# Performance work log

Hardware: AMD Instinct MI355X
Metric: run time of the kernel (lower is better)

The kernel has to match this reference:

```python
import jax, jax.numpy as jnp
import numpy as np

B, Q, D = 4, 8, 128  # batch of volumes, poses per volume, volume side (L == D)


def setup_inputs() -> dict:
    key = jax.random.key(0)
    k1, k2 = jax.random.split(key)
    density = jax.random.normal(k1, (B, D, D, D), dtype=jnp.float32)
    rotation = jax.random.normal(k2, (B, Q, 3, 3), dtype=jnp.float32)
    return {"density": density, "rotation": rotation}


def _project(density, rotation):
    """density: (B, NZ, NY, NX); rotation: (B, Q, 3, 3) -> (B, Q, NY, NX).

    Replicates: rotate an L^3 coord grid, F.grid_sample (trilinear,
    align_corners=True, zero padding), then sum over the last grid axis.
    """
    b, NZ, NY, NX = density.shape
    q = rotation.shape[1]
    L = NZ  # module asserts D == NZ == NY == NX and uses L == D

    lin = jnp.linspace(-1.0, 1.0, L, dtype=density.dtype)
    xx, yy, zz = jnp.meshgrid(lin, lin, lin, indexing="ij")
    coords = jnp.stack([xx, yy, zz], axis=-1)  # (L, L, L, 3)

    Rf = rotation.reshape(b * q, 3, 3)
    # rot_coords[n,i,j,k,m] = sum_c coords[i,j,k,c] * R[n,c,m]
    rc = jnp.einsum("ijkc,ncm->nijkm", coords, Rf)  # (BQ, L, L, L, 3)

    # grid_sample convention: last dim is (x, y, z) indexing (NX, NY, NZ).
    # align_corners=True unnormalization: idx = (c + 1) / 2 * (size - 1)
    x = (rc[..., 0] + 1.0) * 0.5 * (NX - 1)
    y = (rc[..., 1] + 1.0) * 0.5 * (NY - 1)
    z = (rc[..., 2] + 1.0) * 0.5 * (NZ - 1)

    x0 = jnp.floor(x).astype(jnp.int32)
    y0 = jnp.floor(y).astype(jnp.int32)
    z0 = jnp.floor(z).astype(jnp.int32)
    fx = x - x0
    fy = y - y0
    fz = z - z0

    vol = jnp.broadcast_to(density[:, None], (b, q, NZ, NY, NX))
    vol_flat = vol.reshape(b * q, NZ * NY * NX)

    def corner(xc, yc, zc, w):
        valid = (xc >= 0) & (xc < NX) & (yc >= 0) & (yc < NY) & (zc >= 0) & (zc < NZ)
        xi = jnp.clip(xc, 0, NX - 1)
        yi = jnp.clip(yc, 0, NY - 1)
        zi = jnp.clip(zc, 0, NZ - 1)
        idx = (zi * NY + yi) * NX + xi  # (BQ, L, L, L)
        v = jnp.take_along_axis(vol_flat, idx.reshape(b * q, -1), axis=1)
        v = v.reshape(idx.shape)
        return jnp.where(valid, v, 0.0) * w

    sampled = (
        corner(x0,     y0,     z0,     (1 - fx) * (1 - fy) * (1 - fz))
        + corner(x0 + 1, y0,     z0,     fx * (1 - fy) * (1 - fz))
        + corner(x0,     y0 + 1, z0,     (1 - fx) * fy * (1 - fz))
        + corner(x0 + 1, y0 + 1, z0,     fx * fy * (1 - fz))
        + corner(x0,     y0,     z0 + 1, (1 - fx) * (1 - fy) * fz)
        + corner(x0 + 1, y0,     z0 + 1, fx * (1 - fy) * fz)
        + corner(x0,     y0 + 1, z0 + 1, (1 - fx) * fy * fz)
        + corner(x0 + 1, y0 + 1, z0 + 1, fx * fy * fz)
    )  # (BQ, L, L, L) over grid axes (X, Y, Z)

    sampled = sampled.reshape(b, q, L, L, L)
    proj = jnp.sum(sampled.transpose(0, 1, 3, 2, 4), axis=-1)  # (B, Q, L, L)
    return proj


def reference(density, rotation):
    return _project(density, rotation)
```

## Files before the change

kernel.cpp:

```cpp
#include <hip/hip_runtime.h>


#define LSZ 128
#define PACKED_BYTES ((size_t)4 * 128 * 128 * 128 * 8)

typedef unsigned int u4v __attribute__((ext_vector_type(4), aligned(8)));
typedef _Float16 h2 __attribute__((ext_vector_type(2)));

__device__ __forceinline__ h2 ash2(unsigned int u) {
    union { unsigned int u; h2 h; } c; c.u = u; return c.h;
}
__device__ __forceinline__ float dot2(unsigned int pair, h2 w, float acc) {
    return __builtin_amdgcn_fdot2(ash2(pair), w, acc, false);
}
__device__ __forceinline__ h2 pkw(float lo, float hi) {
    auto t = __builtin_amdgcn_cvt_pkrtz(lo, hi);
    union { decltype(t) a; h2 b; } c; c.a = t; return c.b;
}
__device__ __forceinline__ unsigned int pkh(float lo, float hi) {
    auto t = __builtin_amdgcn_cvt_pkrtz(lo, hi);
    union { decltype(t) a; unsigned int u; } c; c.a = t; return c.u;
}

__global__ __launch_bounds__(256) void pack_kernel(
    const float* __restrict__ density, uint2* __restrict__ packed)
{
    const int t  = blockIdx.x * 256 + threadIdx.x;
    const int xq = (t & 31) << 2;
    const int y  = (t >> 5) & 127;
    const int z  = (t >> 12) & 127;
    const int b  = t >> 19;
    const float* __restrict__ v = density + ((size_t)b << 21);
    const int y1 = min(y + 1, 127), z1 = min(z + 1, 127);
    const float4 a0 = *(const float4*)(v + (z  << 14) + (y  << 7) + xq);
    const float4 a1 = *(const float4*)(v + (z  << 14) + (y1 << 7) + xq);
    const float4 c0 = *(const float4*)(v + (z1 << 14) + (y  << 7) + xq);
    const float4 c1 = *(const float4*)(v + (z1 << 14) + (y1 << 7) + xq);
    uint4 o0, o1;
    o0.x = pkh(a0.x, a1.x); o0.y = pkh(c0.x, c1.x);
    o0.z = pkh(a0.y, a1.y); o0.w = pkh(c0.y, c1.y);
    o1.x = pkh(a0.z, a1.z); o1.y = pkh(c0.z, c1.z);
    o1.z = pkh(a0.w, a1.w); o1.w = pkh(c0.w, c1.w);
    uint4* dst = (uint4*)(packed + ((size_t)b << 21) + (z << 14) + (y << 7) + xq);
    dst[0] = o0; dst[1] = o1;
}

#define FPREPI(S, kk) do {                                                    \
    const float kf_ = (float)min((kk), d);                                    \
    const float X_ = fmaf(kf_, R20, Ax);                                      \
    const float Y_ = fmaf(kf_, R21, Ay);                                      \
    const float Z_ = fmaf(kf_, R22, Az);                                      \
    const int ix_ = (int)X_;                                                  \
    const int iy_ = (int)Y_;                                                  \
    const int iz_ = (int)Z_;                                                  \
    fx##S = __builtin_amdgcn_fractf(X_);                                      \
    const float fy_ = __builtin_amdgcn_fractf(Y_);                            \
    fz##S = __builtin_amdgcn_fractf(Z_);                                      \
    hy##S = pkw(1.0f - fy_, fy_);                                             \
    u##S = *(const u4v*)(vol2 + ((iz_ << 14) + (iy_ << 7) + ix_));            \
} while (0)

#define FCONSI(S) do {                                                        \
    const float gx0 = 1.0f - fx##S;                                           \
    const float gz0 = 1.0f - fz##S;                                           \
    const float m00 = dot2(u##S.x, hy##S, 0.0f);                 \
    const float m01 = dot2(u##S.y, hy##S, 0.0f);                 \
    const float m10 = dot2(u##S.z, hy##S, 0.0f);                 \
    const float m11 = dot2(u##S.w, hy##S, 0.0f);                 \
    const float s0_ = fmaf(gx0, m00, fx##S * m10);                            \
    const float s1_ = fmaf(gx0, m01, fx##S * m11);                            \
    acc = fmaf(gz0, s0_, fmaf(fz##S, s1_, acc));                              \
} while (0)

#define SPREP(S, kk) do {                                                     \
    const float kf_ = (float)(kk);                                            \
    const float X_ = fmaf(kf_, R20, Ax);                                      \
    const float Y_ = fmaf(kf_, R21, Ay);                                      \
    const float Z_ = fmaf(kf_, R22, Az);                                      \
    const int ix_ = (int)floorf(X_);                                          \
    const int iy_ = (int)floorf(Y_);                                          \
    const int iz_ = (int)floorf(Z_);                                          \
    const int ex_ = min(max(ix_, 0), 126);                                    \
    const int ey_ = min(max(iy_, 0), 126);                                    \
    const int ez_ = min(max(iz_, 0), 126);                                    \
    u##S = *(const u4v*)(vol2 + ((ez_ << 14) + (ey_ << 7) + ex_));            \
} while (0)

#define SCONS(S, kk) do {                                                     \
    const float kf_ = (float)(kk);                                            \
    const float X_ = fmaf(kf_, R20, Ax);                                      \
    const float Y_ = fmaf(kf_, R21, Ay);                                      \
    const float Z_ = fmaf(kf_, R22, Az);                                      \
    const float xf_ = floorf(X_), yf_ = floorf(Y_), zf_ = floorf(Z_);         \
    const int ix_ = (int)xf_, iy_ = (int)yf_, iz_ = (int)zf_;                 \
    const float fx_ = X_ - xf_, fy_ = Y_ - yf_, fz_ = Z_ - zf_;               \
    const bool vx0_ = (ix_ >= 0)  & (ix_ <= 127);                             \
    const bool vx1_ = (ix_ >= -1) & (ix_ <= 126);                             \
    const bool vy0_ = (iy_ >= 0)  & (iy_ <= 127);                             \
    const bool vy1_ = (iy_ >= -1) & (iy_ <= 126);                             \
    const bool vz0_ = (iz_ >= 0)  & (iz_ <= 127);                             \
    const bool vz1_ = (iz_ >= -1) & (iz_ <= 126);                             \
    const float gx0 = vx0_ ? (1.0f - fx_) : 0.0f;                             \
    const float gx1 = vx1_ ? fx_ : 0.0f;                                      \
    const float gy0 = vy0_ ? (1.0f - fy_) : 0.0f;                             \
    const float gy1 = vy1_ ? fy_ : 0.0f;                                      \
    const float gz0 = vz0_ ? (1.0f - fz_) : 0.0f;                             \
    const float gz1 = vz1_ ? fz_ : 0.0f;                                      \
    const bool xhi_ = (ix_ > 126), xlo_ = (ix_ < 0);                          \
    const bool yhi_ = (iy_ > 126), ylo_ = (iy_ < 0);                          \
    const bool zhi_ = (iz_ > 126), zlo_ = (iz_ < 0);                          \
    const float wlo_ = ylo_ ? gy1 : (yhi_ ? 0.0f : gy0);                      \
    const float whi_ = yhi_ ? gy0 : (ylo_ ? 0.0f : gy1);                      \
    const h2 hy_ = pkw(wlo_, whi_);                                           \
    const unsigned int a0z0 = xhi_ ? u##S.z : u##S.x;                         \
    const unsigned int a0z1 = xhi_ ? u##S.w : u##S.y;                         \
    const unsigned int a1z0 = xlo_ ? u##S.x : u##S.z;                         \
    const unsigned int a1z1 = xlo_ ? u##S.y : u##S.w;                         \
    const unsigned int dA = zhi_ ? a0z1 : a0z0;                  \
    const unsigned int dB = zlo_ ? a0z0 : a0z1;                  \
    const unsigned int dC = zhi_ ? a1z1 : a1z0;                  \
    const unsigned int dD = zlo_ ? a1z0 : a1z1;                  \
    const float m00 = dot2(dA, hy_, 0.0f);                                    \
    const float m01 = dot2(dB, hy_, 0.0f);                                    \
    const float m10 = dot2(dC, hy_, 0.0f);                                    \
    const float m11 = dot2(dD, hy_, 0.0f);                                    \
    const float s0_ = fmaf(gx0, m00, gx1 * m10);                              \
    const float s1_ = fmaf(gx0, m01, gx1 * m11);                              \
    acc = fmaf(gz0, s0_, fmaf(gz1, s1_, acc));                                \
} while (0)

__global__ __launch_bounds__(256) void proj_kernel_packed(
    const uint2* __restrict__ packed,
    const float* __restrict__ rotation,
    float* __restrict__ out)
{
    const int xcd  = blockIdx.x & 7;
    const int slot = blockIdx.x >> 3;
    const int b    = xcd >> 1;
    const int tile = ((xcd & 1) << 8) + slot;
    const int q    = tile >> 6;
    const int blk  = tile & 63;
    const int bq   = (b << 3) + q;

    const int p = (blk << 8) + threadIdx.x;
    const int i = p & (LSZ - 1);
    const int j = p >> 7;

    const float* R = rotation + bq * 9;
    const float R00 = R[0], R01 = R[1], R02 = R[2];
    const float R10 = R[3], R11 = R[4], R12 = R[5];
    const float R20 = R[6], R21 = R[7], R22 = R[8];

    const float step = 2.0f / 127.0f;
    const float li = -1.0f + (float)i * step;
    const float lj = -1.0f + (float)j * step;

    const float Ax = 63.5f * (li * R00 + lj * R10 - R20 + 1.0f);
    const float Ay = 63.5f * (li * R01 + lj * R11 - R21 + 1.0f);
    const float Az = 63.5f * (li * R02 + lj * R12 - R22 + 1.0f);

    float klo = 0.0f, khi = 127.0f;
    float klo2 = 0.0f, khi2 = 127.0f;
    bool empty = false, empty2 = false;
    {
        const float a_[3] = {Ax, Ay, Az};
        const float s_[3] = {R20, R21, R22};
        #pragma unroll
        for (int m = 0; m < 3; ++m) {
            if (fabsf(s_[m]) > 1e-6f) {
                const float r = 1.0f / s_[m];
                const float t0 = (-1.0f   - a_[m]) * r;
                const float t1 = (128.0f  - a_[m]) * r;
                klo = fmaxf(klo, fminf(t0, t1));
                khi = fminf(khi, fmaxf(t0, t1));
                const float w0 = (0.0f    - a_[m]) * r;
                const float w1 = (126.95f - a_[m]) * r;
                klo2 = fmaxf(klo2, fminf(w0, w1));
                khi2 = fminf(khi2, fmaxf(w0, w1));
            } else {
                if (a_[m] <= -1.0f   || a_[m] >= 128.0f)   empty  = true;
                if (a_[m] <  0.001f  || a_[m] >  126.94f)  empty2 = true;
            }
        }
    }
    int a = (int)ceilf(klo - 1e-3f);
    int bnd = (int)floorf(khi + 1e-3f);
    if (a < 0) a = 0;
    if (bnd > 127) bnd = 127;
    if (empty) bnd = a - 1;

    int c = (int)ceilf(klo2 + 0.05f);
    int d = (int)floorf(khi2 - 0.05f);
    if (c < a) c = a;
    if (d > bnd) d = bnd;
    if (empty2 || d < c) { c = bnd + 1; d = bnd; }

    const uint2* __restrict__ vol2 = packed + ((size_t)b << 21);

    float acc = 0.0f;
    u4v uA, uB, uC, uD, uE, uF;
    h2 hyA, hyB, hyC, hyD, hyE, hyF;
    float fxA, fzA, fxB, fzB, fxC, fzC, fxD, fzD, fxE, fzE, fxF, fzF;
    (void)hyA; (void)fxA; (void)fzA;

    {
        int k = a;
        const int e = c - 1;
        if (k <= e) {
            SPREP(A, k);
            while (k <= e) {
                const int kn = k + 1;
                const bool hasB = (kn <= e);
                if (hasB) SPREP(B, kn);
                SCONS(A, k);
                if (hasB) SCONS(B, kn);
                k += 2;
                if (k <= e) SPREP(A, k);
            }
        }
    }

    {
        int n = d - c + 1;
        int k = c;
        if (n > 0) {
            FPREPI(A, k);     FPREPI(B, k + 1); FPREPI(C, k + 2);
            FPREPI(D, k + 3); FPREPI(E, k + 4);
            while (n >= 6) {
                FPREPI(F, k + 5);
                FCONSI(A); FPREPI(A, k + 6);
                FCONSI(B); FPREPI(B, k + 7);
                FCONSI(C); FPREPI(C, k + 8);
                FCONSI(D); FPREPI(D, k + 9);
                FCONSI(E); FPREPI(E, k + 10);
                FCONSI(F);
                k += 6; n -= 6;
            }
            if (n > 0) FCONSI(A);
            if (n > 1) FCONSI(B);
            if (n > 2) FCONSI(C);
            if (n > 3) FCONSI(D);
            if (n > 4) FCONSI(E);
        }
    }

    {
        int k = d + 1;
        const int e = bnd;
        if (k <= e) {
            SPREP(A, k);
            while (k <= e) {
                const int kn = k + 1;
                const bool hasB = (kn <= e);
                if (hasB) SPREP(B, kn);
                SCONS(A, k);
                if (hasB) SCONS(B, kn);
                k += 2;
                if (k <= e) SPREP(A, k);
            }
        }
    }

    out[(bq << 14) + p] = acc;
}

__global__ __launch_bounds__(256) void proj_kernel_fallback(
    const float* __restrict__ density,
    const float* __restrict__ rotation,
    float* __restrict__ out)
{
    const int xcd  = blockIdx.x & 7;
    const int slot = blockIdx.x >> 3;
    const int b    = xcd >> 1;
    const int tile = ((xcd & 1) << 8) + slot;
    const int q    = tile >> 6;
    const int blk  = tile & 63;
    const int bq   = (b << 3) + q;

    const int p = (blk << 8) + threadIdx.x;
    const int i = p & (LSZ - 1);
    const int j = p >> 7;

    const float* R = rotation + bq * 9;
    const float R00 = R[0], R01 = R[1], R02 = R[2];
    const float R10 = R[3], R11 = R[4], R12 = R[5];
    const float R20 = R[6], R21 = R[7], R22 = R[8];

    const float step = 2.0f / 127.0f;
    const float li = -1.0f + (float)i * step;
    const float lj = -1.0f + (float)j * step;

    const float Ax = 63.5f * (li * R00 + lj * R10 - R20 + 1.0f);
    const float Ay = 63.5f * (li * R01 + lj * R11 - R21 + 1.0f);
    const float Az = 63.5f * (li * R02 + lj * R12 - R22 + 1.0f);

    float klo = 0.0f, khi = 127.0f;
    bool empty = false;
    {
        const float a_[3] = {Ax, Ay, Az};
        const float s_[3] = {R20, R21, R22};
        #pragma unroll
        for (int m = 0; m < 3; ++m) {
            if (fabsf(s_[m]) > 1e-6f) {
                const float t0 = (-1.0f  - a_[m]) / s_[m];
                const float t1 = (128.0f - a_[m]) / s_[m];
                klo = fmaxf(klo, fminf(t0, t1));
                khi = fminf(khi, fmaxf(t0, t1));
            } else if (a_[m] <= -1.0f || a_[m] >= 128.0f) {
                empty = true;
            }
        }
    }
    int k_start = (int)ceilf(klo - 1e-3f);
    int k_end   = (int)floorf(khi + 1e-3f);
    if (k_start < 0) k_start = 0;
    if (k_end > 127) k_end = 127;
    if (empty) k_end = k_start - 1;

    const float* __restrict__ vol = density + (size_t)b * (LSZ * LSZ * LSZ);

    float acc = 0.0f;
    for (int k = k_start; k <= k_end; ++k) {
        const float kf = (float)k;
        const float X = fmaf(kf, R20, Ax);
        const float Y = fmaf(kf, R21, Ay);
        const float Z = fmaf(kf, R22, Az);
        const float xf = floorf(X), yf = floorf(Y), zf = floorf(Z);
        const int ix = (int)xf, iy = (int)yf, iz = (int)zf;
        const float fx = X - xf, fy = Y - yf, fz = Z - zf;
        const bool vx0 = (ix >= 0)  & (ix <= 127);
        const bool vx1 = (ix >= -1) & (ix <= 126);
        const bool vy0 = (iy >= 0)  & (iy <= 127);
        const bool vy1 = (iy >= -1) & (iy <= 126);
        const bool vz0 = (iz >= 0)  & (iz <= 127);
        const bool vz1 = (iz >= -1) & (iz <= 126);
        const int cx0 = min(max(ix, 0), 127);
        const int cx1 = min(max(ix + 1, 0), 127);
        const int cy0 = min(max(iy, 0), 127);
        const int cy1 = min(max(iy + 1, 0), 127);
        const int cz0 = min(max(iz, 0), 127);
        const int cz1 = min(max(iz + 1, 0), 127);
        const float gx0 = vx0 ? (1.0f - fx) : 0.0f;
        const float gx1 = vx1 ? fx : 0.0f;
        const float gy0 = vy0 ? (1.0f - fy) : 0.0f;
        const float gy1 = vy1 ? fy : 0.0f;
        const float gz0 = vz0 ? (1.0f - fz) : 0.0f;
        const float gz1 = vz1 ? fz : 0.0f;
        const int z0o = cz0 << 14, z1o = cz1 << 14;
        const int y0o = cy0 << 7,  y1o = cy1 << 7;
        const float v000 = vol[z0o + y0o + cx0];
        const float v100 = vol[z0o + y0o + cx1];
        const float v010 = vol[z0o + y1o + cx0];
        const float v110 = vol[z0o + y1o + cx1];
        const float v001 = vol[z1o + y0o + cx0];
        const float v101 = vol[z1o + y0o + cx1];
        const float v011 = vol[z1o + y1o + cx0];
        const float v111 = vol[z1o + y1o + cx1];
        const float s0 = gy0 * fmaf(gx0, v000, gx1 * v100)
                       + gy1 * fmaf(gx0, v010, gx1 * v110);
        const float s1 = gy0 * fmaf(gx0, v001, gx1 * v101)
                       + gy1 * fmaf(gx0, v011, gx1 * v111);
        acc = fmaf(gz0, s0, fmaf(gz1, s1, acc));
    }

    out[(bq << 14) + p] = acc;
}

extern "C" void kernel_launch(void* const* d_in, const int* in_sizes, int n_in,
                              void* d_out, int out_size, void* d_ws, size_t ws_size,
                              hipStream_t stream) {
    const float* density  = (const float*)d_in[0];
    const float* rotation = (const float*)d_in[1];
    float* out = (float*)d_out;

    if (ws_size >= PACKED_BYTES) {
        uint2* packed = (uint2*)d_ws;
        pack_kernel<<<8192, 256, 0, stream>>>(density, packed);
        proj_kernel_packed<<<2048, 256, 0, stream>>>(packed, rotation, out);
    } else {
        proj_kernel_fallback<<<2048, 256, 0, stream>>>(density, rotation, out);
    }
}
```

Baseline: 213.1 us.

## Map wavefronts to 8x8 pixel tiles and shorten the fast-loop prefetch depth

Each block now covers a 16x16 pixel tile, and each 64-lane wavefront covers an 8x8 sub-tile, replacing the previous layout of two full rows per block. The goal is to make the rotated sample rays of a wavefront touch nearby volume voxels, so gathers hit cache more often and the lanes' loop bounds diverge less. The software prefetch ring in the interior loop shrinks from 6 to 4 stages to lower register pressure. The tail is handled by guarded consumes inside the loop, which may prefetch beyond the valid range and adds branches. The output store becomes a tiled rather than fully coalesced row write.

```diff
diff --git a/kernel.cpp b/kernel.cpp
--- a/kernel.cpp
+++ b/kernel.cpp
@@ -139,12 +139,13 @@
     const int b    = xcd >> 1;
     const int tile = ((xcd & 1) << 8) + slot;
     const int q    = tile >> 6;
-    const int blk  = tile & 63;
+    const int t    = tile & 63;
     const int bq   = (b << 3) + q;
 
-    const int p = (blk << 8) + threadIdx.x;
-    const int i = p & (LSZ - 1);
-    const int j = p >> 7;
+    const int w    = threadIdx.x >> 6;
+    const int lane = threadIdx.x & 63;
+    const int i = ((t & 7) << 4) + ((w & 1) << 3) + (lane & 7);
+    const int j = ((t >> 3) << 4) + ((w >> 1) << 3) + (lane >> 3);
 
     const float* R = rotation + bq * 9;
     const float R00 = R[0], R01 = R[1], R02 = R[2];
@@ -198,9 +199,9 @@
     const uint2* __restrict__ vol2 = packed + ((size_t)b << 21);
 
     float acc = 0.0f;
-    u4v uA, uB, uC, uD, uE, uF;
-    h2 hyA, hyB, hyC, hyD, hyE, hyF;
-    float fxA, fzA, fxB, fzB, fxC, fzC, fxD, fzD, fxE, fzE, fxF, fzF;
+    u4v uA, uB, uC, uD;
+    h2 hyA, hyB, hyC, hyD;
+    float fxA, fzA, fxB, fzB, fxC, fzC, fxD, fzD;
     (void)hyA; (void)fxA; (void)fzA;
 
     {
@@ -224,23 +225,18 @@
         int n = d - c + 1;
         int k = c;
         if (n > 0) {
-            FPREPI(A, k);     FPREPI(B, k + 1); FPREPI(C, k + 2);
-            FPREPI(D, k + 3); FPREPI(E, k + 4);
-            while (n >= 6) {
-                FPREPI(F, k + 5);
-                FCONSI(A); FPREPI(A, k + 6);
-                FCONSI(B); FPREPI(B, k + 7);
-                FCONSI(C); FPREPI(C, k + 8);
-                FCONSI(D); FPREPI(D, k + 9);
-                FCONSI(E); FPREPI(E, k + 10);
-                FCONSI(F);
-                k += 6; n -= 6;
-            }
-            if (n > 0) FCONSI(A);
-            if (n > 1) FCONSI(B);
-            if (n > 2) FCONSI(C);
-            if (n > 3) FCONSI(D);
-            if (n > 4) FCONSI(E);
+            FPREPI(A, k); FPREPI(B, k + 1); FPREPI(C, k + 2);
+            while (n > 0) {
+                FPREPI(D, k + 3);
+                FCONSI(A);
+                FPREPI(A, k + 4);
+                if (n > 1) FCONSI(B);
+                FPREPI(B, k + 5);
+                if (n > 2) FCONSI(C);
+                FPREPI(C, k + 6);
+                if (n > 3) FCONSI(D);
+                k += 4; n -= 4;
+            }
         }
     }
 
@@ -261,7 +257,7 @@
         }
     }
 
-    out[(bq << 14) + p] = acc;
+    out[(bq << 14) + (j << 7) + i] = acc;
 }
 
 __global__ __launch_bounds__(256) void proj_kernel_fallback(
```

Measured after the change: 227.1 us. 6.6% more time.
